# Optimization experiments

Hardware: AMD Instinct MI355X
Metric: run time of the kernel (lower is better)

## Reference

```python
import jax, jax.numpy as jnp
import numpy as np

B, C, L = 2048, 32000, 8
GAMMA = 0.2
BIG = 1e8  # matches torch's 100000000.0 sentinels


def setup_inputs() -> dict:
    key = jax.random.key(0)
    k1, k2, k3 = jax.random.split(key, 3)
    x = jax.random.normal(k1, (B, C), dtype=jnp.float32)
    y = jax.random.randint(k2, (B, L), 0, C, dtype=jnp.int32)
    drop = jax.random.uniform(k3, (B, L)) < 0.3
    drop = drop.at[:, 0].set(False)
    y = jnp.where(drop, -1, y)
    return {"x": x, "y": y}


def reference(x, y):
    b, c = x.shape
    y = y.astype(jnp.int32)
    t = y[:, 0]            # [B] primary targets
    r = y[:, 1:]           # [B, L-1] relative labels, -1 = pad

    # loss1: standard CE(x, t), mean over batch
    logZ = jax.nn.logsumexp(x, axis=1)                       # [B]
    loss1 = jnp.mean(logZ - jnp.take_along_axis(x, t[:, None], axis=1)[:, 0])

    neg_mask = r == -1                                       # [B, L-1]
    sample_mask = jnp.any(~neg_mask, axis=1)                 # [B] rows with >=1 relative

    # min over valid relative logits (argmin+gather in torch == masked min)
    r_safe = jnp.where(neg_mask, 0, r)
    pos_data = jnp.take_along_axis(x, r_safe, axis=1)        # [B, L-1]
    mask_pos_data = jnp.where(neg_mask, BIG, pos_data)
    min_relative = jnp.min(mask_pos_data, axis=1)            # [B]

    # flag: True where class is NOT any of the row's valid labels (incl. target)
    rows = jnp.arange(b, dtype=jnp.int32)[:, None]           # [B,1]
    y_safe = jnp.where(y == -1, 0, y)
    valid = (y != -1).astype(x.dtype)
    mark = jnp.zeros((b, c), x.dtype).at[rows, y_safe].add(valid)
    flag = mark == 0                                         # [B, C]

    new_data = jnp.where(flag, x, -BIG)                      # [B, C]

    # CE over concat([min_relative, new_data], 1) with target 0, per row
    lse = jnp.logaddexp(min_relative, jax.nn.logsumexp(new_data, axis=1))
    loss_row = lse - min_relative                            # [B]

    cnt = jnp.sum(sample_mask.astype(x.dtype))
    loss2 = jnp.sum(jnp.where(sample_mask, loss_row, 0.0)) / jnp.maximum(cnt, 1.0)

    return loss1 + GAMMA * loss2
```

## Files before the change

### kernel.cpp

```cpp
#include <hip/hip_runtime.h>
#include <math.h>

#define B_ROWS 2048
#define C_COLS 32000
#define L_LABELS 8
#define GAMMA_W 0.2f
#define BIG_V 100000000.0f

#define NF4 (C_COLS / 4)
#define TPB 320

__global__ __launch_bounds__(TPB) void
rll_row_kernel(const float* __restrict__ x, const int* __restrict__ y,
               float* __restrict__ partial) {
    const int row = blockIdx.x;
    const int tid = threadIdx.x;
    const float* __restrict__ xr = x + (size_t)row * C_COLS;
    const float4* __restrict__ x4 = reinterpret_cast<const float4*>(xr);

    float s0 = 0.f, s1 = 0.f, s2 = 0.f, s3 = 0.f;

    float4 bufA[16];
    #pragma unroll
    for (int k = 0; k < 16; ++k) bufA[k] = x4[tid + k * TPB];
    #pragma unroll
    for (int k = 0; k < 16; ++k) {
        s0 += __expf(bufA[k].x);
        s1 += __expf(bufA[k].y);
        s2 += __expf(bufA[k].z);
        s3 += __expf(bufA[k].w);
    }

    float4 bufB[9];
    #pragma unroll
    for (int k = 0; k < 9; ++k) bufB[k] = x4[tid + (16 + k) * TPB];
    #pragma unroll
    for (int k = 0; k < 9; ++k) {
        s0 += __expf(bufB[k].x);
        s1 += __expf(bufB[k].y);
        s2 += __expf(bufB[k].z);
        s3 += __expf(bufB[k].w);
    }

    float s = (s0 + s1) + (s2 + s3);

    #pragma unroll
    for (int off = 32; off > 0; off >>= 1) s += __shfl_xor(s, off, 64);

    __shared__ float ss[5];
    if ((tid & 63) == 0) ss[tid >> 6] = s;
    __syncthreads();

    if (tid == 0) {
        s = ((ss[0] + ss[1]) + (ss[2] + ss[3])) + ss[4];
        const float logZ = logf(s);

        const int* __restrict__ yr = y + row * L_LABELS;
        int idx[L_LABELS];
        #pragma unroll
        for (int i = 0; i < L_LABELS; ++i) idx[i] = yr[i];

        float xv[L_LABELS];
        xv[0] = xr[idx[0]];
        float minrel = BIG_V;
        bool any_rel = false;
        #pragma unroll
        for (int i = 1; i < L_LABELS; ++i) {
            if (idx[i] >= 0) {
                float v = xr[idx[i]];
                xv[i] = v;
                minrel = fminf(minrel, v);
                any_rel = true;
            }
        }

        const float loss1_contrib = logZ - xv[0];

        float contrib2 = 0.f, cnt = 0.f;
        if (any_rel) {
            float sub = 0.f;
            #pragma unroll
            for (int i = 0; i < L_LABELS; ++i) {
                const bool vi = (i == 0) || (idx[i] >= 0);
                if (!vi) continue;
                bool dup = false;
                #pragma unroll
                for (int j = 0; j < i; ++j) {
                    const bool vj = (j == 0) || (idx[j] >= 0);
                    if (vj && idx[j] == idx[i]) dup = true;
                }
                if (!dup) sub += expf(xv[i]);
            }
            float s_new = fmaxf(s - sub, 1e-30f);
            const float lse_new = logf(s_new);

            const float a = minrel, b = lse_new;
            const float mx = fmaxf(a, b);
            contrib2 = (mx + log1pf(expf(-fabsf(a - b)))) - a;
            cnt = 1.f;
        }

        partial[row] = loss1_contrib;
        partial[B_ROWS + row] = contrib2;
        partial[2 * B_ROWS + row] = cnt;
    }
}

__global__ __launch_bounds__(1024) void
rll_reduce(const float* __restrict__ p, float* __restrict__ out) {
    const int tid = threadIdx.x;
    float a = p[tid] + p[tid + 1024];
    float b = p[2048 + tid] + p[3072 + tid];
    float c = p[4096 + tid] + p[5120 + tid];

    #pragma unroll
    for (int off = 32; off > 0; off >>= 1) {
        a += __shfl_xor(a, off, 64);
        b += __shfl_xor(b, off, 64);
        c += __shfl_xor(c, off, 64);
    }

    __shared__ float sa[16], sb[16], sc[16];
    const int wave = tid >> 6;
    if ((tid & 63) == 0) { sa[wave] = a; sb[wave] = b; sc[wave] = c; }
    __syncthreads();

    if (tid == 0) {
        float ta = 0.f, tb = 0.f, tc = 0.f;
        #pragma unroll
        for (int w = 0; w < 16; ++w) { ta += sa[w]; tb += sb[w]; tc += sc[w]; }
        const float loss1 = ta / (float)B_ROWS;
        const float loss2 = tb / fmaxf(tc, 1.0f);
        out[0] = loss1 + GAMMA_W * loss2;
    }
}

extern "C" void kernel_launch(void* const* d_in, const int* in_sizes, int n_in,
                              void* d_out, int out_size, void* d_ws, size_t ws_size,
                              hipStream_t stream) {
    const float* x = (const float*)d_in[0];
    const int* yy = (const int*)d_in[1];
    float* out = (float*)d_out;
    float* partial = (float*)d_ws;

    rll_row_kernel<<<B_ROWS, TPB, 0, stream>>>(x, yy, partial);
    rll_reduce<<<1, 1024, 0, stream>>>(partial, out);
}
```

Baseline: 352.1 us.

## Split row sum-exp across five blocks per row with separate per-row finalize kernel

The per-row exp-sum is split across five blocks per row, each reading 1600 float4s, which raises the block count and the memory-level parallelism available across CUs. The per-row label gathers and loss math move into a new kernel with one thread per row, and a third kernel performs the final reduction. This adds one extra launch and a small workspace round trip, and the label gathers in the second kernel become scattered single-thread loads.

```diff
diff --git a/kernel.cpp b/kernel.cpp
--- a/kernel.cpp
+++ b/kernel.cpp
@@ -7,107 +7,112 @@
 #define GAMMA_W 0.2f
 #define BIG_V 100000000.0f
 
-#define NF4 (C_COLS / 4)
-#define TPB 320
+#define TPB1 320
+#define F4T 5
+#define CPR 5
+#define NBLK1 (B_ROWS * CPR)
 
-__global__ __launch_bounds__(TPB) void
-rll_row_kernel(const float* __restrict__ x, const int* __restrict__ y,
-               float* __restrict__ partial) {
-    const int row = blockIdx.x;
+__global__ __launch_bounds__(TPB1) void
+rll_k1_sum(const float* __restrict__ x, float* __restrict__ part) {
+    const int blk = blockIdx.x;
+    const int row = blk / CPR;
+    const int chunk = blk - row * CPR;
     const int tid = threadIdx.x;
-    const float* __restrict__ xr = x + (size_t)row * C_COLS;
-    const float4* __restrict__ x4 = reinterpret_cast<const float4*>(xr);
+    const float4* __restrict__ x4 =
+        reinterpret_cast<const float4*>(x + (size_t)row * C_COLS) + chunk * (TPB1 * F4T);
+
+    float4 buf[F4T];
+    #pragma unroll
+    for (int k = 0; k < F4T; ++k) buf[k] = x4[tid + k * TPB1];
 
     float s0 = 0.f, s1 = 0.f, s2 = 0.f, s3 = 0.f;
-
-    float4 bufA[16];
     #pragma unroll
-    for (int k = 0; k < 16; ++k) bufA[k] = x4[tid + k * TPB];
-    #pragma unroll
-    for (int k = 0; k < 16; ++k) {
-        s0 += __expf(bufA[k].x);
-        s1 += __expf(bufA[k].y);
-        s2 += __expf(bufA[k].z);
-        s3 += __expf(bufA[k].w);
+    for (int k = 0; k < F4T; ++k) {
+        s0 += __expf(buf[k].x);
+        s1 += __expf(buf[k].y);
+        s2 += __expf(buf[k].z);
+        s3 += __expf(buf[k].w);
     }
-
-    float4 bufB[9];
-    #pragma unroll
-    for (int k = 0; k < 9; ++k) bufB[k] = x4[tid + (16 + k) * TPB];
-    #pragma unroll
-    for (int k = 0; k < 9; ++k) {
-        s0 += __expf(bufB[k].x);
-        s1 += __expf(bufB[k].y);
-        s2 += __expf(bufB[k].z);
-        s3 += __expf(bufB[k].w);
-    }
-
     float s = (s0 + s1) + (s2 + s3);
 
     #pragma unroll
     for (int off = 32; off > 0; off >>= 1) s += __shfl_xor(s, off, 64);
 
-    __shared__ float ss[5];
+    __shared__ float ss[TPB1 / 64];
     if ((tid & 63) == 0) ss[tid >> 6] = s;
     __syncthreads();
 
     if (tid == 0) {
-        s = ((ss[0] + ss[1]) + (ss[2] + ss[3])) + ss[4];
-        const float logZ = logf(s);
-
-        const int* __restrict__ yr = y + row * L_LABELS;
-        int idx[L_LABELS];
+        float t = ss[0];
         #pragma unroll
-        for (int i = 0; i < L_LABELS; ++i) idx[i] = yr[i];
-
-        float xv[L_LABELS];
-        xv[0] = xr[idx[0]];
-        float minrel = BIG_V;
-        bool any_rel = false;
-        #pragma unroll
-        for (int i = 1; i < L_LABELS; ++i) {
-            if (idx[i] >= 0) {
-                float v = xr[idx[i]];
-                xv[i] = v;
-                minrel = fminf(minrel, v);
-                any_rel = true;
-            }
-        }
-
-        const float loss1_contrib = logZ - xv[0];
-
-        float contrib2 = 0.f, cnt = 0.f;
-        if (any_rel) {
-            float sub = 0.f;
-            #pragma unroll
-            for (int i = 0; i < L_LABELS; ++i) {
-                const bool vi = (i == 0) || (idx[i] >= 0);
-                if (!vi) continue;
-                bool dup = false;
-                #pragma unroll
-                for (int j = 0; j < i; ++j) {
-                    const bool vj = (j == 0) || (idx[j] >= 0);
-                    if (vj && idx[j] == idx[i]) dup = true;
-                }
-                if (!dup) sub += expf(xv[i]);
-            }
-            float s_new = fmaxf(s - sub, 1e-30f);
-            const float lse_new = logf(s_new);
-
-            const float a = minrel, b = lse_new;
-            const float mx = fmaxf(a, b);
-            contrib2 = (mx + log1pf(expf(-fabsf(a - b)))) - a;
-            cnt = 1.f;
-        }
-
-        partial[row] = loss1_contrib;
-        partial[B_ROWS + row] = contrib2;
-        partial[2 * B_ROWS + row] = cnt;
+        for (int w = 1; w < TPB1 / 64; ++w) t += ss[w];
+        part[blk] = t;
     }
 }
 
+__global__ __launch_bounds__(256) void
+rll_k2_row(const float* __restrict__ x, const int* __restrict__ y,
+           const float* __restrict__ part, float* __restrict__ prow) {
+    const int row = blockIdx.x * 256 + threadIdx.x;
+
+    float s = 0.f;
+    #pragma unroll
+    for (int c = 0; c < CPR; ++c) s += part[row * CPR + c];
+    const float logZ = logf(s);
+
+    const float* __restrict__ xr = x + (size_t)row * C_COLS;
+    const int* __restrict__ yr = y + row * L_LABELS;
+    int idx[L_LABELS];
+    #pragma unroll
+    for (int i = 0; i < L_LABELS; ++i) idx[i] = yr[i];
+
+    float xv[L_LABELS];
+    xv[0] = xr[idx[0]];
+    float minrel = BIG_V;
+    bool any_rel = false;
+    #pragma unroll
+    for (int i = 1; i < L_LABELS; ++i) {
+        if (idx[i] >= 0) {
+            float v = xr[idx[i]];
+            xv[i] = v;
+            minrel = fminf(minrel, v);
+            any_rel = true;
+        }
+    }
+
+    const float loss1_contrib = logZ - xv[0];
+
+    float contrib2 = 0.f, cnt = 0.f;
+    if (any_rel) {
+        float sub = 0.f;
+        #pragma unroll
+        for (int i = 0; i < L_LABELS; ++i) {
+            const bool vi = (i == 0) || (idx[i] >= 0);
+            if (!vi) continue;
+            bool dup = false;
+            #pragma unroll
+            for (int j = 0; j < i; ++j) {
+                const bool vj = (j == 0) || (idx[j] >= 0);
+                if (vj && idx[j] == idx[i]) dup = true;
+            }
+            if (!dup) sub += expf(xv[i]);
+        }
+        float s_new = fmaxf(s - sub, 1e-30f);
+        const float lse_new = logf(s_new);
+
+        const float a = minrel, b = lse_new;
+        const float mx = fmaxf(a, b);
+        contrib2 = (mx + log1pf(expf(-fabsf(a - b)))) - a;
+        cnt = 1.f;
+    }
+
+    prow[row] = loss1_contrib;
+    prow[B_ROWS + row] = contrib2;
+    prow[2 * B_ROWS + row] = cnt;
+}
+
 __global__ __launch_bounds__(1024) void
-rll_reduce(const float* __restrict__ p, float* __restrict__ out) {
+rll_k3_reduce(const float* __restrict__ p, float* __restrict__ out) {
     const int tid = threadIdx.x;
     float a = p[tid] + p[tid + 1024];
     float b = p[2048 + tid] + p[3072 + tid];
@@ -141,8 +146,10 @@
     const float* x = (const float*)d_in[0];
     const int* yy = (const int*)d_in[1];
     float* out = (float*)d_out;
-    float* partial = (float*)d_ws;
+    float* part = (float*)d_ws;
+    float* prow = part + NBLK1;
 
-    rll_row_kernel<<<B_ROWS, TPB, 0, stream>>>(x, yy, partial);
-    rll_reduce<<<1, 1024, 0, stream>>>(partial, out);
+    rll_k1_sum<<<NBLK1, TPB1, 0, stream>>>(x, part);
+    rll_k2_row<<<B_ROWS / 256, 256, 0, stream>>>(x, yy, part, prow);
+    rll_k3_reduce<<<1, 1024, 0, stream>>>(prow, out);
 }
```

Measured after the change: 356.1 us. About the same (+1.1%).
